# Optimization experiments

Hardware: AMD Instinct MI355X
Metric: run time of the kernel (lower is better)

## Reference

```python
import jax, jax.numpy as jnp
import numpy as np

EPS = 1e-6
ENERGY_THRESHOLD = 0.95
LS_INIT = 1e-5


def setup_inputs() -> dict:
    key = jax.random.key(0)
    k_x, k_u, k_s, k_v = jax.random.split(key, 4)
    dim, max_rank = 4096, 16
    x = jax.random.normal(k_x, (4, 2048, dim), dtype=jnp.float32)
    U = jax.random.normal(k_u, (dim, max_rank), dtype=jnp.float32) * 0.02
    S = jax.random.uniform(k_s, (max_rank,), dtype=jnp.float32)
    V = jax.random.normal(k_v, (max_rank, dim), dtype=jnp.float32) * 0.02
    norm_weight = jnp.ones((dim,), dtype=jnp.float32)
    gamma = jnp.full((dim,), LS_INIT, dtype=jnp.float32)
    return {"x": x, "U": U, "S": S, "V": V,
            "norm_weight": norm_weight, "gamma": gamma}


def _rank_mask(S):
    # Effective rank from singular-value energy (non-differentiable decision,
    # matching torch's .item() host sync which detaches it from autograd).
    s_abs = jnp.abs(S)
    cum = jnp.cumsum(s_abs) / jnp.maximum(s_abs.sum(), 1e-8)
    hit = cum >= ENERGY_THRESHOLD
    r = jnp.where(hit.any(), jnp.argmax(hit) + 1, S.shape[0])
    keep = (jnp.arange(S.shape[0]) < r).astype(S.dtype)
    return jax.lax.stop_gradient(keep)


def reference(x, U, S, V, norm_weight, gamma):
    # RMSNorm (computed in fp32, matching x.float() in torch)
    xf = x.astype(jnp.float32)
    x_norm = (xf * jax.lax.rsqrt(jnp.mean(xf * xf, axis=-1, keepdims=True) + EPS)).astype(x.dtype)
    x_norm = x_norm * norm_weight
    # Adaptive-rank low-rank projection: masking columns >= r equals slicing [:r]
    keep = _rank_mask(S)
    h = jnp.einsum('bsd,dr->bsr', x_norm, U)        # [B,S,max_rank]
    h = h * (S * keep)                               # zero out ranks >= r
    h = jnp.einsum('bsr,rd->bsd', h, V)             # [B,S,dim]
    # LayerScale + residual
    return x + h * gamma
```

## Files before the change

### kernel.cpp

```cpp
#include <hip/hip_runtime.h>

#define DIM   4096
#define RANK  16
#define BM    16
#define NT    512
#define NWAVE 8
#define KTILE 512
#define NTILE (DIM/KTILE)
#define XPAD  516
#define NCB   (DIM/16/NWAVE)

typedef __fp16 f16;
typedef __fp16 half4 __attribute__((ext_vector_type(4)));
typedef __fp16 half8 __attribute__((ext_vector_type(8)));
typedef float  floatx4 __attribute__((ext_vector_type(4)));

#define VM_WAIT0 { asm volatile("s_waitcnt vmcnt(0)" ::: "memory"); \
                   __builtin_amdgcn_sched_barrier(0); }

__device__ __forceinline__ void gld16(const void* g, void* l) {
    __builtin_amdgcn_global_load_lds((__attribute__((address_space(1))) void*)g,
                                     (__attribute__((address_space(3))) void*)l,
                                     16, 0, 0);
}

__global__ __launch_bounds__(256) void prep_weights(const float* __restrict__ U,
    const float* __restrict__ nw, const float* __restrict__ V,
    f16* __restrict__ Ub, f16* __restrict__ Vb)
{
    const int i   = blockIdx.x * 256 + threadIdx.x;
    const int l   = i & 63;
    const int n   = l & 15;
    const int blk = l >> 4;
    if (i < 8192) {
        const int kb = i >> 6;
        half8 u;
        #pragma unroll
        for (int e = 0; e < 8; ++e) {
            const int k = kb * 32 + blk * 8 + e;
            u[e] = (f16)(nw[k] * U[(size_t)k * RANK + n]);
        }
        *(half8*)(Ub + (size_t)i * 8) = u;
    }
    {
        const int cb = i >> 6;
        half4 v;
        #pragma unroll
        for (int e = 0; e < 4; ++e) {
            const int k = blk * 4 + e;
            v[e] = (f16)V[(size_t)k * DIM + cb * 16 + n];
        }
        *(half4*)(Vb + (size_t)i * 4) = v;
    }
}

__global__ __launch_bounds__(NT, 4) void arl_fused(
    const float* __restrict__ x,  const f16* __restrict__ Ub,
    const f16* __restrict__ Vb,   const float* __restrict__ S,
    const float* __restrict__ gamma, float* __restrict__ out)
{
    const int t   = threadIdx.x;
    const int w   = t >> 6;
    const int l   = t & 63;
    const int n   = l & 15;
    const int blk = l >> 4;
    const size_t row0 = (size_t)blockIdx.x * BM;

    __shared__ __align__(16) float xbuf[2][BM][XPAD];
    __shared__ float s_hacc[NWAVE][16][17];
    __shared__ float s_ssq[NWAVE][16];
    __shared__ __align__(8) f16 s_hh[16][16];

    const float* xg   = x + row0 * DIM;
    const int    srow = 2 * w;

    floatx4 acc = {0.f, 0.f, 0.f, 0.f};
    float ssq = 0.f;

    #pragma unroll
    for (int j = 0; j < 4; ++j) {
        const int row  = srow + (j >> 1);
        const int half = j & 1;
        gld16(xg + (size_t)row * DIM + half * 256 + l * 4,
              &xbuf[0][row][half * 256]);
    }

    int cur = 0;
    #pragma unroll 1
    for (int tt = 0; tt < NTILE; ++tt) {
        VM_WAIT0;
        __syncthreads();
        if (tt + 1 < NTILE) {
            #pragma unroll
            for (int j = 0; j < 4; ++j) {
                const int row  = srow + (j >> 1);
                const int half = j & 1;
                gld16(xg + (size_t)row * DIM + (size_t)(tt + 1) * KTILE
                          + half * 256 + l * 4,
                      &xbuf[cur ^ 1][row][half * 256]);
            }
        }
        #pragma unroll
        for (int s = 0; s < 2; ++s) {
            const int koff = w * 64 + s * 32 + blk * 8;
            const float4 xa0 = *(const float4*)&xbuf[cur][n][koff];
            const float4 xa1 = *(const float4*)&xbuf[cur][n][koff + 4];
            const int kb = tt * (KTILE / 32) + w * 2 + s;
            const half8 ub = *(const half8*)(Ub + ((size_t)kb * 64 + l) * 8);
            ssq = fmaf(xa0.x, xa0.x, ssq); ssq = fmaf(xa0.y, xa0.y, ssq);
            ssq = fmaf(xa0.z, xa0.z, ssq); ssq = fmaf(xa0.w, xa0.w, ssq);
            ssq = fmaf(xa1.x, xa1.x, ssq); ssq = fmaf(xa1.y, xa1.y, ssq);
            ssq = fmaf(xa1.z, xa1.z, ssq); ssq = fmaf(xa1.w, xa1.w, ssq);
            half8 a;
            a[0] = (f16)xa0.x; a[1] = (f16)xa0.y; a[2] = (f16)xa0.z; a[3] = (f16)xa0.w;
            a[4] = (f16)xa1.x; a[5] = (f16)xa1.y; a[6] = (f16)xa1.z; a[7] = (f16)xa1.w;
            acc = __builtin_amdgcn_mfma_f32_16x16x32_f16(a, ub, acc, 0, 0, 0);
        }
        cur ^= 1;
    }

    ssq += __shfl_xor(ssq, 16, 64);
    ssq += __shfl_xor(ssq, 32, 64);
    if (l < 16) s_ssq[w][l] = ssq;

    #pragma unroll
    for (int j = 0; j < 4; ++j) s_hacc[w][blk * 4 + j][n] = acc[j];
    __syncthreads();

    if (t < 256) {
        const int m = t >> 4, q = t & 15;
        float hsum = 0.f, tssq = 0.f;
        #pragma unroll
        for (int ww = 0; ww < NWAVE; ++ww) {
            hsum += s_hacc[ww][m][q];
            tssq += s_ssq[ww][m];
        }
        const float rstd = rsqrtf(tssq * (1.0f / DIM) + 1e-6f);
        float tot = 0.f;
        #pragma unroll
        for (int i = 0; i < RANK; ++i) tot += fabsf(S[i]);
        const float denom = fmaxf(tot, 1e-8f);
        float cum = 0.f, se = 0.f;
        #pragma unroll
        for (int i = 0; i < RANK; ++i) {
            if (i == q) se = ((cum / denom) < 0.95f) ? S[i] : 0.f;
            cum += fabsf(S[i]);
        }
        s_hh[m][q] = (f16)(hsum * se * rstd);
    }
    __syncthreads();

    const half4 ah = *(const half4*)&s_hh[n][blk * 4];
    const half4* Vb4 = (const half4*)Vb;
    const floatx4 zero = {0.f, 0.f, 0.f, 0.f};
    const float* xrow = x   + (row0 + n) * DIM;
    float*       orow = out + (row0 + n) * DIM;

    #pragma unroll 4
    for (int i = 0; i < NCB; ++i) {
        const int cb = w * NCB + i;
        const int c0 = cb * 16 + blk * 4;
        const half4 bv = Vb4[(size_t)cb * 64 + l];
        floatx4 d = __builtin_amdgcn_mfma_f32_16x16x16f16(bv, ah, zero, 0, 0, 0);
        const float4 g  = *(const float4*)(gamma + c0);
        const float4 xv = *(const float4*)(xrow + c0);
        floatx4 o;
        o[0] = fmaf(g.x, d[0], xv.x);
        o[1] = fmaf(g.y, d[1], xv.y);
        o[2] = fmaf(g.z, d[2], xv.z);
        o[3] = fmaf(g.w, d[3], xv.w);
        __builtin_nontemporal_store(o, (floatx4*)(orow + c0));
    }
}

extern "C" void kernel_launch(void* const* d_in, const int* in_sizes, int n_in,
                              void* d_out, int out_size, void* d_ws, size_t ws_size,
                              hipStream_t stream) {
    (void)in_sizes; (void)n_in; (void)ws_size;
    const float* x  = (const float*)d_in[0];
    const float* U  = (const float*)d_in[1];
    const float* S  = (const float*)d_in[2];
    const float* V  = (const float*)d_in[3];
    const float* nw = (const float*)d_in[4];
    const float* g  = (const float*)d_in[5];
    float* out = (float*)d_out;
    f16* Ub = (f16*)d_ws;
    f16* Vb = (f16*)((char*)d_ws + 128 * 1024);

    hipLaunchKernelGGL(prep_weights, dim3(64), dim3(256), 0, stream,
                       U, nw, V, Ub, Vb);

    const int rows = out_size / DIM;
    const int grid = rows / BM;
    hipLaunchKernelGGL(arl_fused, dim3(grid), dim3(NT), 0, stream,
                       x, Ub, Vb, S, g, out);
}
```

Measured before the change: 84.05 us.

## Give each wave its own K-slice ring buffer, removing per-tile block barriers

Each wave now streams its own contiguous 512-column slice of the 16 rows through a private double-buffered LDS ring, using XOR-swizzled addresses. This removes the per-tile __syncthreads and lets waves run out of step with each other. It also waits with partial vmcnt counts so the U-weight loads can stay in flight. The LDS footprint shrinks, and the barrier-free design depends on each wave only reading data it loaded itself.

```diff
diff --git a/kernel.cpp b/kernel.cpp
--- a/kernel.cpp
+++ b/kernel.cpp
@@ -5,18 +5,16 @@
 #define BM    16
 #define NT    512
 #define NWAVE 8
-#define KTILE 512
-#define NTILE (DIM/KTILE)
-#define XPAD  516
-#define NCB   (DIM/16/NWAVE)
+#define NST   8
 
 typedef __fp16 f16;
 typedef __fp16 half4 __attribute__((ext_vector_type(4)));
 typedef __fp16 half8 __attribute__((ext_vector_type(8)));
 typedef float  floatx4 __attribute__((ext_vector_type(4)));
 
-#define VM_WAIT0 { asm volatile("s_waitcnt vmcnt(0)" ::: "memory"); \
-                   __builtin_amdgcn_sched_barrier(0); }
+#define VM_WAIT(N) { asm volatile("s_waitcnt vmcnt(" #N ")" ::: "memory"); \
+                     __builtin_amdgcn_sched_barrier(0); }
+#define SCHED_FENCE() __builtin_amdgcn_sched_barrier(0)
 
 __device__ __forceinline__ void gld16(const void* g, void* l) {
     __builtin_amdgcn_global_load_lds((__attribute__((address_space(1))) void*)g,
@@ -66,47 +64,49 @@
     const int blk = l >> 4;
     const size_t row0 = (size_t)blockIdx.x * BM;
 
-    __shared__ __align__(16) float xbuf[2][BM][XPAD];
+    __shared__ __align__(16) float ring[NWAVE][2][BM * 64];
     __shared__ float s_hacc[NWAVE][16][17];
     __shared__ float s_ssq[NWAVE][16];
     __shared__ __align__(8) f16 s_hh[16][16];
 
-    const float* xg   = x + row0 * DIM;
-    const int    srow = 2 * w;
+    const float* xg = x + row0 * DIM + w * 512;
 
     floatx4 acc = {0.f, 0.f, 0.f, 0.f};
     float ssq = 0.f;
 
     #pragma unroll
     for (int j = 0; j < 4; ++j) {
-        const int row  = srow + (j >> 1);
-        const int half = j & 1;
-        gld16(xg + (size_t)row * DIM + half * 256 + l * 4,
-              &xbuf[0][row][half * 256]);
+        const int rl  = 4 * j + (l >> 4);
+        const int gsw = (l & 15) ^ (rl & 7);
+        gld16(xg + (size_t)rl * DIM + gsw * 4, &ring[w][0][j * 256]);
     }
 
-    int cur = 0;
     #pragma unroll 1
-    for (int tt = 0; tt < NTILE; ++tt) {
-        VM_WAIT0;
-        __syncthreads();
-        if (tt + 1 < NTILE) {
+    for (int st = 0; st < NST; ++st) {
+        const int kb0 = w * 16 + st * 2;
+        const half8 ub0 = *(const half8*)(Ub + ((size_t)kb0 * 64 + l) * 8);
+        const half8 ub1 = *(const half8*)(Ub + ((size_t)(kb0 + 1) * 64 + l) * 8);
+        SCHED_FENCE();
+        if (st + 1 < NST) {
             #pragma unroll
             for (int j = 0; j < 4; ++j) {
-                const int row  = srow + (j >> 1);
-                const int half = j & 1;
-                gld16(xg + (size_t)row * DIM + (size_t)(tt + 1) * KTILE
-                          + half * 256 + l * 4,
-                      &xbuf[cur ^ 1][row][half * 256]);
+                const int rl  = 4 * j + (l >> 4);
+                const int gsw = (l & 15) ^ (rl & 7);
+                gld16(xg + (size_t)rl * DIM + (st + 1) * 64 + gsw * 4,
+                      &ring[w][(st + 1) & 1][j * 256]);
             }
+            VM_WAIT(6)
+        } else {
+            VM_WAIT(2)
         }
+
+        const float* buf = ring[w][st & 1];
         #pragma unroll
         for (int s = 0; s < 2; ++s) {
-            const int koff = w * 64 + s * 32 + blk * 8;
-            const float4 xa0 = *(const float4*)&xbuf[cur][n][koff];
-            const float4 xa1 = *(const float4*)&xbuf[cur][n][koff + 4];
-            const int kb = tt * (KTILE / 32) + w * 2 + s;
-            const half8 ub = *(const half8*)(Ub + ((size_t)kb * 64 + l) * 8);
+            const int g0 = (s * 8 + blk * 2)     ^ (n & 7);
+            const int g1 = (s * 8 + blk * 2 + 1) ^ (n & 7);
+            const float4 xa0 = *(const float4*)&buf[n * 64 + g0 * 4];
+            const float4 xa1 = *(const float4*)&buf[n * 64 + g1 * 4];
             ssq = fmaf(xa0.x, xa0.x, ssq); ssq = fmaf(xa0.y, xa0.y, ssq);
             ssq = fmaf(xa0.z, xa0.z, ssq); ssq = fmaf(xa0.w, xa0.w, ssq);
             ssq = fmaf(xa1.x, xa1.x, ssq); ssq = fmaf(xa1.y, xa1.y, ssq);
@@ -114,9 +114,8 @@
             half8 a;
             a[0] = (f16)xa0.x; a[1] = (f16)xa0.y; a[2] = (f16)xa0.z; a[3] = (f16)xa0.w;
             a[4] = (f16)xa1.x; a[5] = (f16)xa1.y; a[6] = (f16)xa1.z; a[7] = (f16)xa1.w;
-            acc = __builtin_amdgcn_mfma_f32_16x16x32_f16(a, ub, acc, 0, 0, 0);
+            acc = __builtin_amdgcn_mfma_f32_16x16x32_f16(a, s ? ub1 : ub0, acc, 0, 0, 0);
         }
-        cur ^= 1;
     }
 
     ssq += __shfl_xor(ssq, 16, 64);
@@ -157,8 +156,8 @@
     float*       orow = out + (row0 + n) * DIM;
 
     #pragma unroll 4
-    for (int i = 0; i < NCB; ++i) {
-        const int cb = w * NCB + i;
+    for (int i = 0; i < 32; ++i) {
+        const int cb = w * 32 + i;
         const int c0 = cb * 16 + blk * 4;
         const half4 bv = Vb4[(size_t)cb * 64 + l];
         floatx4 d = __builtin_amdgcn_mfma_f32_16x16x16f16(bv, ah, zero, 0, 0, 0);
```

After: 74.65 us. 1.13x faster.
